# Kernel optimization log

Hardware: AMD Instinct MI355X
Metric: run time of the kernel (lower is better)

Reference implementation:

```python
import jax, jax.numpy as jnp
import numpy as np

N, T, F = 4096, 24, 16          # nodes, seq_len, in_features
H = 128                          # temporal_hidden
NH, DO = 4, 32                   # gat num_heads, gat out_features (NH*DO == H)
SEM, PH = 64, 32                 # semantic hidden, predictor hidden
SLOPE = 0.2                      # leaky_relu negative slope
ADJ_P = 0.01                     # adjacency density


def setup_inputs() -> dict:
    key = jax.random.key(0)
    ks = jax.random.split(key, 40)
    f32 = jnp.float32

    def rn(k, shape, s=0.02):
        return jax.random.normal(k, shape, f32) * s

    features = jax.random.normal(ks[0], (N, T, F), f32)
    pos_adj = (jax.random.uniform(ks[1], (N, N)) < ADJ_P).astype(f32)
    neg_adj = (jax.random.uniform(ks[2], (N, N)) < ADJ_P).astype(f32)

    inp = dict(features=features, pos_adj=pos_adj, neg_adj=neg_adj)
    # GRU (torch layout: W_ih [3H,F], W_hh [3H,H], gate order r,z,n)
    inp['gru_Wih'] = rn(ks[3], (3 * H, F), 1.0 / np.sqrt(H))
    inp['gru_Whh'] = rn(ks[4], (3 * H, H), 1.0 / np.sqrt(H))
    inp['gru_bih'] = rn(ks[5], (3 * H,), 1.0 / np.sqrt(H))
    inp['gru_bhh'] = rn(ks[6], (3 * H,), 1.0 / np.sqrt(H))
    # GAT params (linear weights stored [in, out] so we use x @ W)
    i = 7
    for pre in ('pos', 'neg'):
        inp[pre + '_W'] = rn(ks[i], (H, NH * DO)); i += 1
        inp[pre + '_u'] = rn(ks[i], (NH, DO, 1), 1.0); i += 1
        inp[pre + '_v'] = rn(ks[i], (NH, DO, 1), 1.0); i += 1
        inp[pre + '_b'] = rn(ks[i], (1, NH * DO)); i += 1
        inp[pre + '_pW'] = rn(ks[i], (H, NH * DO)); i += 1
        inp[pre + '_pb'] = jnp.zeros((NH * DO,), f32)
    inp['self_W'] = rn(ks[i], (H, H)); i += 1
    inp['self_b'] = jnp.zeros((H,), f32)
    inp['mpos_W'] = rn(ks[i], (NH * DO, H)); i += 1
    inp['mpos_b'] = jnp.zeros((H,), f32)
    inp['mneg_W'] = rn(ks[i], (NH * DO, H)); i += 1
    inp['mneg_b'] = jnp.zeros((H,), f32)
    inp['sem_W1'] = rn(ks[i], (H, SEM)); i += 1
    inp['sem_b1'] = jnp.zeros((SEM,), f32)
    inp['sem_W2'] = rn(ks[i], (SEM, 1)); i += 1
    inp['pred_W1'] = rn(ks[i], (H, PH)); i += 1
    inp['pred_b1'] = jnp.zeros((PH,), f32)
    inp['pred_W2'] = rn(ks[i], (PH, 1)); i += 1
    inp['pred_b2'] = jnp.zeros((1,), f32)
    return inp


def _gru_last(x, Wih, Whh, bih, bhh):
    # x: [N, T, F] -> last hidden state [N, H]
    gi_all = jnp.einsum('ntf,gf->tng', x, Wih) + bih  # precompute input gates [T,N,3H]
    h0 = jnp.zeros((x.shape[0], Whh.shape[1]), x.dtype)

    def step(h, gi):
        gh = h @ Whh.T + bhh
        ir, iz, in_ = jnp.split(gi, 3, axis=-1)
        hr, hz, hn = jnp.split(gh, 3, axis=-1)
        r = jax.nn.sigmoid(ir + hr)
        z = jax.nn.sigmoid(iz + hz)
        n = jnp.tanh(in_ + r * hn)
        return (1.0 - z) * n + z * h, None

    h, _ = jax.lax.scan(step, h0, gi_all)
    return h


def _gat(x, adj, W, u, v, b, pW, pb):
    sup = (x @ W).reshape(-1, NH, DO).transpose(1, 0, 2)     # [NH, N, DO]
    f1 = jnp.matmul(sup, u).reshape(NH, 1, -1)               # [NH, 1, N]
    f2 = jnp.matmul(sup, v).reshape(NH, -1, 1)               # [NH, N, 1]
    w = jax.nn.leaky_relu(f1 + f2, SLOPE)                    # [NH, N, N]
    mw = w * adj                                             # mask
    rs = mw.sum(axis=2, keepdims=True)
    rs = jnp.where(rs == 0, jnp.ones_like(rs), rs)
    attn = mw / rs
    out = jnp.matmul(attn, sup).transpose(1, 0, 2).reshape(-1, NH * DO)
    return out + b + x @ pW + pb                             # bias + residual


def _pairnorm_si(x):
    x = x - x.mean(axis=0)
    rn = jnp.sqrt(1e-6 + (x * x).sum(axis=1, keepdims=True))
    return x / rn


def reference(features, pos_adj, neg_adj,
              gru_Wih, gru_Whh, gru_bih, gru_bhh,
              pos_W, pos_u, pos_v, pos_b, pos_pW, pos_pb,
              neg_W, neg_u, neg_v, neg_b, neg_pW, neg_pb,
              self_W, self_b, mpos_W, mpos_b, mneg_W, mneg_b,
              sem_W1, sem_b1, sem_W2,
              pred_W1, pred_b1, pred_W2, pred_b2):
    support = _gru_last(features, gru_Wih, gru_Whh, gru_bih, gru_bhh)  # [N, H]
    pos_sup = _gat(support, pos_adj, pos_W, pos_u, pos_v, pos_b, pos_pW, pos_pb)
    neg_sup = _gat(support, neg_adj, neg_W, neg_u, neg_v, neg_b, neg_pW, neg_pb)
    self_e = support @ self_W + self_b
    pos_e = pos_sup @ mpos_W + mpos_b
    neg_e = neg_sup @ mneg_W + mneg_b
    emb = jnp.stack([self_e, pos_e, neg_e], axis=1)          # [N, 3, H]
    w = jnp.tanh(emb @ sem_W1 + sem_b1) @ sem_W2             # [N, 3, 1]
    beta = jax.nn.softmax(w, axis=1)
    fused = (beta * emb).sum(axis=1)                          # [N, H]
    fused = _pairnorm_si(fused)
    h = jax.nn.relu(fused @ pred_W1 + pred_b1)               # dropout is eval no-op
    out = jax.nn.sigmoid(h @ pred_W2 + pred_b2).squeeze(-1)  # [N]
    return out
```

## Files before the change

kernel.cpp:

```cpp
#include <hip/hip_runtime.h>


#define NN 4096

typedef unsigned short u16;
typedef unsigned int   u32;
typedef unsigned long long u64;
typedef __attribute__((ext_vector_type(8))) short  short8;
typedef __attribute__((ext_vector_type(4))) float  float4v;

__device__ inline float bf2f(u16 u){ return __uint_as_float(((u32)u)<<16); }
__device__ inline u16 f2bf(float f){
  u32 x = __float_as_uint(f);
  return (u16)((x + 0x7fffu + ((x>>16)&1u))>>16);
}
__device__ inline float ldm(const void* p, int i, int bf){
  return bf ? bf2f(((const u16*)p)[i]) : ((const float*)p)[i];
}
__device__ inline u16 ldm16(const void* p, int i, int bf){
  return bf ? ((const u16*)p)[i] : f2bf(((const float*)p)[i]);
}
__device__ inline float fexp(float x){
  x = fminf(fmaxf(x,-80.f),80.f);
  return __builtin_amdgcn_exp2f(x*1.4426950408889634f);
}
__device__ inline float sigm(float x){
  return __builtin_amdgcn_rcpf(1.f + fexp(-x));
}
__device__ inline float tanhf_(float x){
  float c = fminf(fmaxf(x,-15.f),15.f);
  float e = __builtin_amdgcn_exp2f(c*2.8853900817779268f);
  return (e-1.f)*__builtin_amdgcn_rcpf(e+1.f);
}
__device__ inline float4v mfma16(short8 a, short8 b, float4v c){
  return __builtin_amdgcn_mfma_f32_16x16x32_bf16(a,b,c,0,0,0);
}

__global__ __launch_bounds__(256) void k_detect(const u32* __restrict__ adj,
                                                int* __restrict__ mflag)
{
  int i = (blockIdx.x*256 + threadIdx.x)*4;
  uint4 v = *(const uint4*)(adj + i);
  u32 acc = (v.x | v.y | v.z | v.w) & 0xFFFFu;
  unsigned long long b = __ballot(acc != 0);
  if ((threadIdx.x & 63) == 0 && b) atomicOr(mflag, 1);
}

__global__ __launch_bounds__(256) void k_imp(
  const int* __restrict__ mflag,
  const void* gWih, const void* gWhh, const void* gbih, const void* gbhh,
  const void* posW, const void* posu, const void* posv, const void* posb,
  const void* pospW, const void* pospb,
  const void* negW, const void* negu, const void* negv, const void* negb,
  const void* negpW, const void* negpb,
  const void* selfW, const void* selfb, const void* mposW, const void* mposb,
  const void* mnegW, const void* mnegb,
  const void* semW1, const void* semb1, const void* semW2,
  const void* predW1, const void* predb1, const void* predW2, const void* predb2,
  u16* __restrict__ Wihb, u16* __restrict__ Whhb,
  u16* __restrict__ WT1,  u16* __restrict__ WT2,
  float* __restrict__ cbrz, float* __restrict__ cbin, float* __restrict__ cbhn,
  float* __restrict__ cuv,  float* __restrict__ cgb,  float* __restrict__ csb,
  float* __restrict__ cw1,  float* __restrict__ cb1,  float* __restrict__ cw2,
  float* __restrict__ cpw1, float* __restrict__ cpb1, float* __restrict__ cpw2,
  float* __restrict__ cpb2)
{
  const int bf = mflag[0];
  int i = blockIdx.x*256 + threadIdx.x;
  if (i < 6144){ Wihb[i]=ldm16(gWih,i,bf); return; }  i-=6144;
  if (i < 49152){ Whhb[i]=ldm16(gWhh,i,bf); return; } i-=49152;
  if (i < 81920){
    int m=i>>7,k=i&127,sel=m>>7,ml=m&127;
    const void* s = sel==0?posW: sel==1?pospW: sel==2?negW: sel==3?negpW: selfW;
    WT1[i]=ldm16(s,k*128+ml,bf); return;
  } i-=81920;
  if (i < 32768){
    int m=i>>7,k=i&127;
    const void* s = (m<128)? mposW : mnegW;
    WT2[i]=ldm16(s,k*128+(m&127),bf); return;
  } i-=32768;
  if (i < 256){ cbrz[i]=ldm(gbih,i,bf)+ldm(gbhh,i,bf); return; } i-=256;
  if (i < 128){ cbin[i]=ldm(gbih,256+i,bf); return; } i-=128;
  if (i < 128){ cbhn[i]=ldm(gbhh,256+i,bf); return; } i-=128;
  if (i < 512){
    int s=i>>8, rem=i&255, wh=rem>>7, hd=rem&127;
    const void* p = s? (wh? negv:negu) : (wh? posv:posu);
    cuv[i]=ldm(p,hd,bf); return;
  } i-=512;
  if (i < 256){
    int s=i>>7, d=i&127;
    cgb[i]=ldm(s?negb:posb,d,bf)+ldm(s?negpb:pospb,d,bf); return;
  } i-=256;
  if (i < 384){
    int t=i>>7, d=i&127;
    const void* p = t==0? selfb : t==1? mposb : mnegb;
    csb[i]=ldm(p,d,bf); return;
  } i-=384;
  if (i < 8192){ cw1[i]=ldm(semW1,i,bf); return; } i-=8192;
  if (i < 64){ cb1[i]=ldm(semb1,i,bf); return; } i-=64;
  if (i < 64){ cw2[i]=ldm(semW2,i,bf); return; } i-=64;
  if (i < 4096){ cpw1[i]=ldm(predW1,i,bf); return; } i-=4096;
  if (i < 32){ cpb1[i]=ldm(predb1,i,bf); return; } i-=32;
  if (i < 32){ cpw2[i]=ldm(predW2,i,bf); return; } i-=32;
  if (i < 1){ cpb2[i]=ldm(predb2,i,bf); return; }
}

__global__ __launch_bounds__(256) void k_csr(
  const int* __restrict__ mflag,
  const void* posadj, const void* negadj,
  int* __restrict__ deg, u16* __restrict__ idx)
{
  const int bf = mflag[0];
  const int s = blockIdx.y;
  const void* adj = s? negadj : posadj;
  const int lane = threadIdx.x&63;
  const int hr   = blockIdx.x*4 + (threadIdx.x>>6);
  const int row  = hr>>1, half = hr&1;
  u32 mask = 0;
  if (bf){
    const u16* rp = (const u16*)adj + (size_t)row*4096 + half*2048;
    #pragma unroll
    for (int q=0;q<4;q++){
      uint4 v = *(const uint4*)(rp + q*512 + lane*8);
      if (v.x&0xffffu) mask|=1u<<(q*8+0); if (v.x>>16) mask|=1u<<(q*8+1);
      if (v.y&0xffffu) mask|=1u<<(q*8+2); if (v.y>>16) mask|=1u<<(q*8+3);
      if (v.z&0xffffu) mask|=1u<<(q*8+4); if (v.z>>16) mask|=1u<<(q*8+5);
      if (v.w&0xffffu) mask|=1u<<(q*8+6); if (v.w>>16) mask|=1u<<(q*8+7);
    }
  } else {
    const float* rp = (const float*)adj + (size_t)row*4096 + half*2048;
    #pragma unroll
    for (int q=0;q<8;q++){
      uint4 v = *(const uint4*)(rp + q*256 + lane*4);
      if (v.x) mask|=1u<<(q*4+0);
      if (v.y) mask|=1u<<(q*4+1);
      if (v.z) mask|=1u<<(q*4+2);
      if (v.w) mask|=1u<<(q*4+3);
    }
  }
  int cnt = __popc(mask);
  int pre = cnt;
  #pragma unroll
  for (int off=1; off<64; off<<=1){
    int o = __shfl_up(pre, off);
    if (lane>=off) pre += o;
  }
  int tot = __shfl(pre, 63);
  int wbase = 0;
  if (lane==0) wbase = atomicAdd(&deg[s*NN+row], tot);
  wbase = __shfl(wbase, 0);
  int base_p = wbase + pre - cnt;
  u16* out = idx + ((size_t)s*NN + row)*128;
  u32 mm = mask; int k = 0;
  while (mm){
    int b = __ffs(mm)-1; mm &= mm-1;
    int e = bf ? (half*2048 + (b>>3)*512 + lane*8 + (b&7))
               : (half*2048 + (b>>2)*256 + lane*4 + (b&3));
    int p = base_p + k; k++;
    if (p<128) out[p] = (u16)e;
  }
}

__global__ __launch_bounds__(512) void k_gru(
  const int* __restrict__ mflag, const void* feat,
  const u16* __restrict__ Wihb, const u16* __restrict__ Whhb,
  const float* __restrict__ cbrz, const float* __restrict__ cbin,
  const float* __restrict__ cbhn, u16* __restrict__ supb)
{
  __shared__ __attribute__((aligned(16))) u16 sh_x[16*392];
  __shared__ __attribute__((aligned(16))) u16 hbuf[2][16*136];

  const int tid=threadIdx.x, lane=tid&63, wv=tid>>6;
  const int quad=lane>>4, c15=lane&15;
  const int n0=blockIdx.x*16;
  const int bf=mflag[0];

  if (bf){
    const u16* f16p=(const u16*)feat;
    for (int i=tid;i<16*384;i+=512){ int n=i/384,e=i-n*384; sh_x[n*392+e]=f16p[(size_t)(n0+n)*384+e]; }
  } else {
    const float* f32p=(const float*)feat;
    for (int i=tid;i<16*384;i+=512){ int n=i/384,e=i-n*384; sh_x[n*392+e]=f2bf(f32p[(size_t)(n0+n)*384+e]); }
  }
  for (int i=tid;i<16*136;i+=512) hbuf[0][i]=0;

  const short8 z8={0,0,0,0,0,0,0,0};
  const float4v z4={0.f,0.f,0.f,0.f};

  short8 bh[3][4], bx[3];
  #pragma unroll
  for (int g=0;g<3;g++){
    int rowb=(g*8+wv)*16+c15;
    #pragma unroll
    for (int ks=0;ks<4;ks++) bh[g][ks]=*(const short8*)(Whhb+(size_t)rowb*128+ks*32+quad*8);
    bx[g] = (quad<2)? *(const short8*)(Wihb+(size_t)rowb*16+quad*8) : z8;
  }

  const int j0=wv*16+c15;
  const float brz_r=cbrz[j0], brz_z=cbrz[128+j0];
  const float bin0=cbin[j0],  bhn0=cbhn[j0];

  float hr[4]={0.f,0.f,0.f,0.f};

  __syncthreads();

  for (int t=0;t<24;t++){
    const u16* hb  = hbuf[t&1];
    u16*       hbn = hbuf[(t+1)&1];
    short8 ah[4];
    #pragma unroll
    for (int ks=0;ks<4;ks++) ah[ks]=*(const short8*)(hb + c15*136 + ks*32 + quad*8);
    short8 ax = (quad<2)? *(const short8*)(sh_x + c15*392 + t*16 + quad*8) : z8;

    float4v racc = mfma16(ax,bx[0],z4);
    float4v zacc = mfma16(ax,bx[1],z4);
    float4v ni   = mfma16(ax,bx[2],z4);
    float4v nh   = z4;
    #pragma unroll
    for (int ks=0;ks<4;ks++){
      racc = mfma16(ah[ks],bh[0][ks],racc);
      zacc = mfma16(ah[ks],bh[1][ks],zacc);
      nh   = mfma16(ah[ks],bh[2][ks],nh);
    }
    #pragma unroll
    for (int rr=0;rr<4;rr++){
      const int node = quad*4+rr;
      float r_ = sigm(racc[rr]+brz_r);
      float z_ = sigm(zacc[rr]+brz_z);
      float n_ = tanhf_(ni[rr]+bin0 + r_*(nh[rr]+bhn0));
      float hv = (1.f-z_)*n_ + z_*hr[rr];
      hr[rr]=hv; hbn[node*136+j0]=f2bf(hv);
    }
    __syncthreads();
  }
  #pragma unroll
  for (int rr=0;rr<4;rr++){
    const int node=quad*4+rr;
    supb[(size_t)(n0+node)*128+j0]=f2bf(hr[rr]);
  }
}

__global__ __launch_bounds__(256) void k_lin1(
  const u16* __restrict__ supb, const u16* __restrict__ WT1,
  const float* __restrict__ cuv, float* __restrict__ C1,
  float* __restrict__ f12)
{
  __shared__ __attribute__((aligned(16))) u16 sA[16*136];
  const int tid=threadIdx.x, lane=tid&63, wv=tid>>6, quad=lane>>4, c15=lane&15;
  const int n0=blockIdx.x*16;
  for (int i=tid;i<2048;i+=256){ int n=i>>7,k=i&127; sA[n*136+k]=supb[(size_t)(n0+n)*128+k]; }
  __syncthreads();
  short8 a[4];
  #pragma unroll
  for (int ks=0;ks<4;ks++) a[ks]=*(const short8*)(sA+c15*136+ks*32+quad*8);
  for (int q=0;q<10;q++){
    int tile=wv*10+q;
    float4v acc={0.f,0.f,0.f,0.f};
    #pragma unroll
    for (int ks=0;ks<4;ks++){
      short8 b=*(const short8*)(WT1+(size_t)(tile*16+c15)*128+ks*32+quad*8);
      acc=mfma16(a[ks],b,acc);
    }
    #pragma unroll
    for (int r=0;r<4;r++) C1[(size_t)(n0+quad*4+r)*640 + tile*16 + c15]=acc[r];
  }
  __syncthreads();
  for (int q=tid; q<512; q+=256){
    int nl=q&15, h=(q>>4)&3, wsel=(q>>6)&1, s=(q>>7)&1;
    const float* uvp = cuv + s*256 + wsel*128 + h*32;
    const float* SL  = C1 + (size_t)(n0+nl)*640 + s*256 + h*32;
    float t=0.f;
    #pragma unroll
    for (int d=0;d<32;d++) t += SL[d]*uvp[d];
    f12[s*32768 + wsel*16384 + h*4096 + (n0+nl)] = t;
  }
}

__global__ __launch_bounds__(256) void k_gat(
  const float* __restrict__ C1, const float* __restrict__ f12,
  const int* __restrict__ deg, const u16* __restrict__ idx,
  const float* __restrict__ cgb, u16* __restrict__ spnb)
{
  __shared__ u16   nbuf[4][128];
  __shared__ float wbuf[4][4][128];
  const int s=blockIdx.y;
  const int wv=threadIdx.x>>6;
  const int i=blockIdx.x*4 + wv;
  const int lane=threadIdx.x&63;
  const int d0=lane, d1=lane+64, h0=lane>>5, h1=2+(lane>>5);
  const float* f1 = f12 + s*32768;
  const float* f2 = f12 + s*32768 + 16384;
  const int dgr = deg[s*NN+i];
  const int dg  = dgr>128 ? 128 : dgr;
  const u16* nb = idx + ((size_t)s*NN+i)*128;
  ((u32*)nbuf[wv])[lane] = ((const u32*)nb)[lane];
  float f2v[4];
  #pragma unroll
  for (int h=0;h<4;h++) f2v[h]=f2[h*4096+i];
  for (int e=lane; e<dg; e+=64){
    int j = nbuf[wv][e];
    #pragma unroll
    for (int h=0;h<4;h++){
      float w = f1[h*4096+j] + f2v[h];
      wbuf[wv][h][e] = w>0.f ? w : 0.2f*w;
    }
  }
  float acc0=0.f,acc1=0.f,rs0=0.f,rs1=0.f;
  for (int e=0;e<dg;e++){
    float w0 = wbuf[wv][h0][e];
    float w1 = wbuf[wv][h1][e];
    int j = nbuf[wv][e];
    const float* SL = C1 + (size_t)j*640 + s*256;
    acc0 += w0*SL[d0]; rs0 += w0;
    acc1 += w1*SL[d1]; rs1 += w1;
  }
  if (rs0==0.f) rs0=1.f;
  if (rs1==0.f) rs1=1.f;
  const float* P = C1 + (size_t)i*640 + s*256 + 128;
  float o0 = acc0/rs0 + cgb[s*128+d0] + P[d0];
  float o1 = acc1/rs1 + cgb[s*128+d1] + P[d1];
  size_t o = ((size_t)s*NN + i)*128;
  spnb[o+d0]=f2bf(o0); spnb[o+d1]=f2bf(o1);
}

__global__ __launch_bounds__(256) void k_lin2(
  const u16* __restrict__ spnb, const u16* __restrict__ WT2, float* __restrict__ E)
{
  const int s=blockIdx.y;
  __shared__ __attribute__((aligned(16))) u16 sA[16*136];
  const int tid=threadIdx.x, lane=tid&63, wv=tid>>6, quad=lane>>4, c15=lane&15;
  const int n0=blockIdx.x*16;
  const u16* A = spnb + (size_t)s*NN*128;
  for (int i=tid;i<2048;i+=256){ int n=i>>7,k=i&127; sA[n*136+k]=A[(size_t)(n0+n)*128+k]; }
  __syncthreads();
  short8 a[4];
  #pragma unroll
  for (int ks=0;ks<4;ks++) a[ks]=*(const short8*)(sA+c15*136+ks*32+quad*8);
  #pragma unroll
  for (int q=0;q<2;q++){
    int tile=wv*2+q;
    float4v acc={0.f,0.f,0.f,0.f};
    #pragma unroll
    for (int ks=0;ks<4;ks++){
      short8 b=*(const short8*)(WT2+(size_t)(s*128+tile*16+c15)*128+ks*32+quad*8);
      acc=mfma16(a[ks],b,acc);
    }
    #pragma unroll
    for (int r=0;r<4;r++) E[(size_t)(n0+quad*4+r)*256 + s*128 + tile*16 + c15]=acc[r];
  }
}

__global__ __launch_bounds__(256) void k_sem(
  const float* __restrict__ C1, const float* __restrict__ E,
  const float* __restrict__ csb, const float* __restrict__ cw1,
  const float* __restrict__ cb1, const float* __restrict__ cw2,
  float* __restrict__ fused)
{
  __shared__ float sW1[128*64];
  __shared__ float sW2[64];
  __shared__ float sb1[64];
  __shared__ float sE[4][3][128];
  const int tid=threadIdx.x, wv=tid>>6, lane=tid&63;
  for (int i=tid;i<8192;i+=256) sW1[i]=cw1[i];
  if (tid<64){ sW2[tid]=cw2[tid]; sb1[tid]=cb1[tid]; }
  const int n = blockIdx.x*4 + wv;
  for (int d=lane; d<128; d+=64){
    sE[wv][0][d] = C1[(size_t)n*640+512+d] + csb[d];
    sE[wv][1][d] = E[(size_t)n*256 + d]    + csb[128+d];
    sE[wv][2][d] = E[(size_t)n*256+128+d]  + csb[256+d];
  }
  __syncthreads();
  float sc[3];
  #pragma unroll
  for (int s=0;s<3;s++){
    float t = sb1[lane];
    for (int k=0;k<128;k++) t += sE[wv][s][k]*sW1[k*64+lane];
    t = tanhf_(t);
    float p = t*sW2[lane];
    #pragma unroll
    for (int off=32; off; off>>=1) p += __shfl_xor(p, off);
    sc[s]=p;
  }
  float mx = fmaxf(sc[0], fmaxf(sc[1],sc[2]));
  float e0=fexp(sc[0]-mx), e1=fexp(sc[1]-mx), e2=fexp(sc[2]-mx);
  float inv = 1.f/(e0+e1+e2);
  float b0=e0*inv, b1=e1*inv, b2=e2*inv;
  for (int d=lane; d<128; d+=64)
    fused[(size_t)n*128+d] = b0*sE[wv][0][d] + b1*sE[wv][1][d] + b2*sE[wv][2][d];
}

__global__ __launch_bounds__(256) void k_mean(const float* __restrict__ fused,
                                              float* __restrict__ meanacc)
{
  const int d = threadIdx.x & 127, h2 = threadIdx.x >> 7;
  const int n0 = blockIdx.x*128;
  float s=0.f;
  for (int n=n0+h2; n<n0+128; n+=2) s += fused[(size_t)n*128+d];
  __shared__ float red[256];
  red[threadIdx.x]=s; __syncthreads();
  if (threadIdx.x<128) atomicAdd(&meanacc[threadIdx.x], red[threadIdx.x]+red[threadIdx.x+128]);
}

__global__ __launch_bounds__(256) void k_pred(
  const float* __restrict__ fused, const float* __restrict__ meanacc,
  const float* __restrict__ cpw1, const float* __restrict__ cpb1,
  const float* __restrict__ cpw2, const float* __restrict__ cpb2,
  float* __restrict__ out)
{
  __shared__ float sy[4][128];
  __shared__ float sW1[128*32];
  __shared__ float sW2[32];
  const int tid=threadIdx.x, wv=tid>>6, lane=tid&63;
  for (int i=tid;i<4096;i+=256) sW1[i]=cpw1[i];
  if (tid<32) sW2[tid]=cpw2[tid];
  const int n = blockIdx.x*4 + wv;
  const float inv_n = 1.f/4096.f;
  float x0 = fused[(size_t)n*128+lane]    - meanacc[lane]*inv_n;
  float x1 = fused[(size_t)n*128+64+lane] - meanacc[64+lane]*inv_n;
  float ss = x0*x0 + x1*x1;
  #pragma unroll
  for (int o=32;o;o>>=1) ss += __shfl_xor(ss,o);
  float ir = 1.f/sqrtf(1e-6f + ss);
  sy[wv][lane]=x0*ir; sy[wv][64+lane]=x1*ir;
  __syncthreads();
  float h=0.f;
  if (lane<32){
    h = cpb1[lane];
    for (int k=0;k<128;k++) h += sy[wv][k]*sW1[k*32+lane];
    h = h>0.f? h : 0.f;
    h = h*sW2[lane];
  }
  #pragma unroll
  for (int o=32;o;o>>=1) h += __shfl_xor(h,o);
  if (!lane){
    float z = h + cpb2[0];
    out[n] = __builtin_amdgcn_rcpf(1.f + fexp(-z));
  }
}

extern "C" void kernel_launch(void* const* d_in, const int* in_sizes, int n_in,
                              void* d_out, int out_size, void* d_ws, size_t ws_size,
                              hipStream_t stream)
{
  const void* feat  =d_in[0];
  const void* posadj=d_in[1];
  const void* negadj=d_in[2];
  const void* gWih  =d_in[3];
  const void* gWhh  =d_in[4];
  const void* gbih  =d_in[5];
  const void* gbhh  =d_in[6];
  const void* posW  =d_in[7];
  const void* posu  =d_in[8];
  const void* posv  =d_in[9];
  const void* posb  =d_in[10];
  const void* pospW =d_in[11];
  const void* pospb =d_in[12];
  const void* negW  =d_in[13];
  const void* negu  =d_in[14];
  const void* negv  =d_in[15];
  const void* negb  =d_in[16];
  const void* negpW =d_in[17];
  const void* negpb =d_in[18];
  const void* selfW =d_in[19];
  const void* selfb =d_in[20];
  const void* mposW =d_in[21];
  const void* mposb =d_in[22];
  const void* mnegW =d_in[23];
  const void* mnegb =d_in[24];
  const void* semW1 =d_in[25];
  const void* semb1 =d_in[26];
  const void* semW2 =d_in[27];
  const void* predW1=d_in[28];
  const void* predb1=d_in[29];
  const void* predW2=d_in[30];
  const void* predb2=d_in[31];

  char* wsb=(char*)d_ws; size_t off=0;
  auto alloc=[&](size_t bytes)->void*{ void* p=wsb+off; off+=(bytes+255)&~(size_t)255; return p; };
  int*   mflag=(int*)  alloc(256);
  u16*   Wihb =(u16*)  alloc(6144*2);
  u16*   Whhb =(u16*)  alloc(49152*2);
  u16*   WT1  =(u16*)  alloc(81920*2);
  u16*   WT2  =(u16*)  alloc(32768*2);
  float* cbrz =(float*)alloc(256*4);
  float* cbin =(float*)alloc(128*4);
  float* cbhn =(float*)alloc(128*4);
  float* cuv  =(float*)alloc(512*4);
  float* cgb  =(float*)alloc(256*4);
  float* csb  =(float*)alloc(384*4);
  float* cw1  =(float*)alloc(8192*4);
  float* cb1  =(float*)alloc(64*4);
  float* cw2  =(float*)alloc(64*4);
  float* cpw1 =(float*)alloc(4096*4);
  float* cpb1 =(float*)alloc(32*4);
  float* cpw2 =(float*)alloc(32*4);
  float* cpb2 =(float*)alloc(4);
  u16*   supb =(u16*)  alloc((size_t)NN*128*2);
  float* C1   =(float*)alloc((size_t)NN*640*4);
  float* f12  =(float*)alloc((size_t)65536*4);
  int*   deg  =(int*)  alloc((size_t)2*NN*4);
  u16*   nidx =(u16*)  alloc((size_t)2*NN*128*2);
  u16*   spnb =(u16*)  alloc((size_t)2*NN*128*2);
  float* E    =(float*)alloc((size_t)NN*256*4);
  float* fused=(float*)alloc((size_t)NN*128*4);
  float* meanacc=(float*)alloc(128*4);
  (void)ws_size; (void)in_sizes; (void)n_in; (void)out_size;

  hipMemsetAsync(mflag, 0, 4, stream);
  hipMemsetAsync(deg, 0, (size_t)2*NN*4, stream);
  hipMemsetAsync(meanacc, 0, 128*4, stream);
  k_detect<<<16,             256,0,stream>>>((const u32*)posadj,mflag);
  k_imp   <<<720,            256,0,stream>>>(mflag,gWih,gWhh,gbih,gbhh,
              posW,posu,posv,posb,pospW,pospb,negW,negu,negv,negb,negpW,negpb,
              selfW,selfb,mposW,mposb,mnegW,mnegb,semW1,semb1,semW2,
              predW1,predb1,predW2,predb2,
              Wihb,Whhb,WT1,WT2,cbrz,cbin,cbhn,cuv,cgb,csb,cw1,cb1,cw2,
              cpw1,cpb1,cpw2,cpb2);
  k_csr <<<dim3(2048,2),     256,0,stream>>>(mflag,posadj,negadj,deg,nidx);
  k_gru <<<NN/16,            512,0,stream>>>(mflag,feat,Wihb,Whhb,cbrz,cbin,cbhn,supb);
  k_lin1<<<NN/16,            256,0,stream>>>(supb,WT1,cuv,C1,f12);
  k_gat <<<dim3(NN/4,2),     256,0,stream>>>(C1,f12,deg,nidx,cgb,spnb);
  k_lin2<<<dim3(NN/16,2),    256,0,stream>>>(spnb,WT2,E);
  k_sem <<<NN/4,             256,0,stream>>>(C1,E,csb,cw1,cb1,cw2,fused);
  k_mean<<<32,               256,0,stream>>>(fused,meanacc);
  k_pred<<<NN/4,             256,0,stream>>>(fused,meanacc,cpw1,cpb1,cpw2,cpb2,(float*)d_out);
}
```

Baseline: 321.3 us.

## Fuse kernels: CSR build with GRU+lin1, GAT with lin2, mean into sem

```diff
diff --git a/kernel.cpp b/kernel.cpp
--- a/kernel.cpp
+++ b/kernel.cpp
@@ -35,15 +35,25 @@
 __device__ inline float4v mfma16(short8 a, short8 b, float4v c){
   return __builtin_amdgcn_mfma_f32_16x16x32_bf16(a,b,c,0,0,0);
 }
+__device__ inline int rdbf(const int* __restrict__ mflag){
+  int b=0;
+  #pragma unroll
+  for (int k=0;k<16;k++) b|=mflag[k];
+  return b;
+}
 
 __global__ __launch_bounds__(256) void k_detect(const u32* __restrict__ adj,
                                                 int* __restrict__ mflag)
 {
+  __shared__ u32 w4[4];
+  const int lane=threadIdx.x&63, wv=threadIdx.x>>6;
   int i = (blockIdx.x*256 + threadIdx.x)*4;
   uint4 v = *(const uint4*)(adj + i);
   u32 acc = (v.x | v.y | v.z | v.w) & 0xFFFFu;
   unsigned long long b = __ballot(acc != 0);
-  if ((threadIdx.x & 63) == 0 && b) atomicOr(mflag, 1);
+  if (lane==0) w4[wv] = (b!=0);
+  __syncthreads();
+  if (threadIdx.x==0) mflag[blockIdx.x] = (w4[0]|w4[1]|w4[2]|w4[3]) ? 1 : 0;
 }
 
 __global__ __launch_bounds__(256) void k_imp(
@@ -63,9 +73,9 @@
   float* __restrict__ cuv,  float* __restrict__ cgb,  float* __restrict__ csb,
   float* __restrict__ cw1,  float* __restrict__ cb1,  float* __restrict__ cw2,
   float* __restrict__ cpw1, float* __restrict__ cpb1, float* __restrict__ cpw2,
-  float* __restrict__ cpb2)
-{
-  const int bf = mflag[0];
+  float* __restrict__ cpb2, float* __restrict__ meanacc)
+{
+  const int bf = rdbf(mflag);
   int i = blockIdx.x*256 + threadIdx.x;
   if (i < 6144){ Wihb[i]=ldm16(gWih,i,bf); return; }  i-=6144;
   if (i < 49152){ Whhb[i]=ldm16(gWhh,i,bf); return; } i-=49152;
@@ -102,78 +112,79 @@
   if (i < 4096){ cpw1[i]=ldm(predW1,i,bf); return; } i-=4096;
   if (i < 32){ cpb1[i]=ldm(predb1,i,bf); return; } i-=32;
   if (i < 32){ cpw2[i]=ldm(predW2,i,bf); return; } i-=32;
-  if (i < 1){ cpb2[i]=ldm(predb2,i,bf); return; }
-}
-
-__global__ __launch_bounds__(256) void k_csr(
+  if (i < 1){ cpb2[i]=ldm(predb2,i,bf); return; } i-=1;
+  if (i < 128){ meanacc[i]=0.f; return; }
+}
+
+__global__ __launch_bounds__(512) void k_fat1(
   const int* __restrict__ mflag,
   const void* posadj, const void* negadj,
-  int* __restrict__ deg, u16* __restrict__ idx)
-{
-  const int bf = mflag[0];
-  const int s = blockIdx.y;
-  const void* adj = s? negadj : posadj;
-  const int lane = threadIdx.x&63;
-  const int hr   = blockIdx.x*4 + (threadIdx.x>>6);
-  const int row  = hr>>1, half = hr&1;
-  u32 mask = 0;
-  if (bf){
-    const u16* rp = (const u16*)adj + (size_t)row*4096 + half*2048;
-    #pragma unroll
-    for (int q=0;q<4;q++){
-      uint4 v = *(const uint4*)(rp + q*512 + lane*8);
-      if (v.x&0xffffu) mask|=1u<<(q*8+0); if (v.x>>16) mask|=1u<<(q*8+1);
-      if (v.y&0xffffu) mask|=1u<<(q*8+2); if (v.y>>16) mask|=1u<<(q*8+3);
-      if (v.z&0xffffu) mask|=1u<<(q*8+4); if (v.z>>16) mask|=1u<<(q*8+5);
-      if (v.w&0xffffu) mask|=1u<<(q*8+6); if (v.w>>16) mask|=1u<<(q*8+7);
-    }
-  } else {
-    const float* rp = (const float*)adj + (size_t)row*4096 + half*2048;
-    #pragma unroll
-    for (int q=0;q<8;q++){
-      uint4 v = *(const uint4*)(rp + q*256 + lane*4);
-      if (v.x) mask|=1u<<(q*4+0);
-      if (v.y) mask|=1u<<(q*4+1);
-      if (v.z) mask|=1u<<(q*4+2);
-      if (v.w) mask|=1u<<(q*4+3);
-    }
-  }
-  int cnt = __popc(mask);
-  int pre = cnt;
-  #pragma unroll
-  for (int off=1; off<64; off<<=1){
-    int o = __shfl_up(pre, off);
-    if (lane>=off) pre += o;
-  }
-  int tot = __shfl(pre, 63);
-  int wbase = 0;
-  if (lane==0) wbase = atomicAdd(&deg[s*NN+row], tot);
-  wbase = __shfl(wbase, 0);
-  int base_p = wbase + pre - cnt;
-  u16* out = idx + ((size_t)s*NN + row)*128;
-  u32 mm = mask; int k = 0;
-  while (mm){
-    int b = __ffs(mm)-1; mm &= mm-1;
-    int e = bf ? (half*2048 + (b>>3)*512 + lane*8 + (b&7))
-               : (half*2048 + (b>>2)*256 + lane*4 + (b&3));
-    int p = base_p + k; k++;
-    if (p<128) out[p] = (u16)e;
-  }
-}
-
-__global__ __launch_bounds__(512) void k_gru(
-  const int* __restrict__ mflag, const void* feat,
+  int* __restrict__ deg, u16* __restrict__ idx,
+  const void* feat,
   const u16* __restrict__ Wihb, const u16* __restrict__ Whhb,
   const float* __restrict__ cbrz, const float* __restrict__ cbin,
-  const float* __restrict__ cbhn, u16* __restrict__ supb)
+  const float* __restrict__ cbhn,
+  const u16* __restrict__ WT1, const float* __restrict__ cuv,
+  float* __restrict__ C1, float* __restrict__ f12)
 {
   __shared__ __attribute__((aligned(16))) u16 sh_x[16*392];
   __shared__ __attribute__((aligned(16))) u16 hbuf[2][16*136];
-
+  const int bf = rdbf(mflag);
   const int tid=threadIdx.x, lane=tid&63, wv=tid>>6;
+  const int bx=blockIdx.x;
+
+  if (bx < 1024){
+    const int gid = bx*8 + wv;
+    const int s = gid>>12, row = gid&4095;
+    const void* adj = s? negadj : posadj;
+    u64 mask = 0;
+    if (bf){
+      const u16* rp = (const u16*)adj + (size_t)row*4096;
+      #pragma unroll
+      for (int it=0; it<8; it++){
+        const uint4 vv = *(const uint4*)(rp + it*512 + lane*8);
+        u32 w[4]={vv.x,vv.y,vv.z,vv.w};
+        #pragma unroll
+        for (int q=0;q<4;q++){
+          if (w[q]&0xffffu) mask |= 1ull<<(it*8+2*q);
+          if (w[q]>>16)     mask |= 1ull<<(it*8+2*q+1);
+        }
+      }
+    } else {
+      const float* rp = (const float*)adj + (size_t)row*4096;
+      #pragma unroll
+      for (int it=0; it<16; it++){
+        const uint4 vv = *(const uint4*)(rp + it*256 + lane*4);
+        if (vv.x) mask |= 1ull<<(it*4+0);
+        if (vv.y) mask |= 1ull<<(it*4+1);
+        if (vv.z) mask |= 1ull<<(it*4+2);
+        if (vv.w) mask |= 1ull<<(it*4+3);
+      }
+    }
+    int cnt = __popcll(mask);
+    int pre = cnt;
+    #pragma unroll
+    for (int off=1; off<64; off<<=1){
+      int o = __shfl_up(pre, off);
+      if (lane>=off) pre += o;
+    }
+    int base_p = pre - cnt;
+    int total = __shfl(pre, 63);
+    u16* out = idx + ((size_t)s*NN + row)*128;
+    u64 mm = mask; int k = 0;
+    while (mm){
+      int b = __ffsll(mm)-1; mm &= mm-1;
+      int e = bf ? ((b>>3)*512 + lane*8 + (b&7))
+                 : ((b>>2)*256 + lane*4 + (b&3));
+      int p = base_p + k; k++;
+      if (p<128) out[p] = (u16)e;
+    }
+    if (lane==0) deg[s*NN+row] = total>128 ? 128 : total;
+    return;
+  }
+
   const int quad=lane>>4, c15=lane&15;
-  const int n0=blockIdx.x*16;
-  const int bf=mflag[0];
+  const int n0=(bx-1024)*16;
 
   if (bf){
     const u16* f16p=(const u16*)feat;
@@ -186,22 +197,18 @@
 
   const short8 z8={0,0,0,0,0,0,0,0};
   const float4v z4={0.f,0.f,0.f,0.f};
-
-  short8 bh[3][4], bx[3];
+  short8 bh[3][4], bx3[3];
   #pragma unroll
   for (int g=0;g<3;g++){
     int rowb=(g*8+wv)*16+c15;
     #pragma unroll
     for (int ks=0;ks<4;ks++) bh[g][ks]=*(const short8*)(Whhb+(size_t)rowb*128+ks*32+quad*8);
-    bx[g] = (quad<2)? *(const short8*)(Wihb+(size_t)rowb*16+quad*8) : z8;
-  }
-
+    bx3[g] = (quad<2)? *(const short8*)(Wihb+(size_t)rowb*16+quad*8) : z8;
+  }
   const int j0=wv*16+c15;
   const float brz_r=cbrz[j0], brz_z=cbrz[128+j0];
   const float bin0=cbin[j0],  bhn0=cbhn[j0];
-
   float hr[4]={0.f,0.f,0.f,0.f};
-
   __syncthreads();
 
   for (int t=0;t<24;t++){
@@ -211,10 +218,9 @@
     #pragma unroll
     for (int ks=0;ks<4;ks++) ah[ks]=*(const short8*)(hb + c15*136 + ks*32 + quad*8);
     short8 ax = (quad<2)? *(const short8*)(sh_x + c15*392 + t*16 + quad*8) : z8;
-
-    float4v racc = mfma16(ax,bx[0],z4);
-    float4v zacc = mfma16(ax,bx[1],z4);
-    float4v ni   = mfma16(ax,bx[2],z4);
+    float4v racc = mfma16(ax,bx3[0],z4);
+    float4v zacc = mfma16(ax,bx3[1],z4);
+    float4v ni   = mfma16(ax,bx3[2],z4);
     float4v nh   = z4;
     #pragma unroll
     for (int ks=0;ks<4;ks++){
@@ -233,28 +239,12 @@
     }
     __syncthreads();
   }
-  #pragma unroll
-  for (int rr=0;rr<4;rr++){
-    const int node=quad*4+rr;
-    supb[(size_t)(n0+node)*128+j0]=f2bf(hr[rr]);
-  }
-}
-
-__global__ __launch_bounds__(256) void k_lin1(
-  const u16* __restrict__ supb, const u16* __restrict__ WT1,
-  const float* __restrict__ cuv, float* __restrict__ C1,
-  float* __restrict__ f12)
-{
-  __shared__ __attribute__((aligned(16))) u16 sA[16*136];
-  const int tid=threadIdx.x, lane=tid&63, wv=tid>>6, quad=lane>>4, c15=lane&15;
-  const int n0=blockIdx.x*16;
-  for (int i=tid;i<2048;i+=256){ int n=i>>7,k=i&127; sA[n*136+k]=supb[(size_t)(n0+n)*128+k]; }
-  __syncthreads();
   short8 a[4];
   #pragma unroll
-  for (int ks=0;ks<4;ks++) a[ks]=*(const short8*)(sA+c15*136+ks*32+quad*8);
-  for (int q=0;q<10;q++){
-    int tile=wv*10+q;
+  for (int ks=0;ks<4;ks++) a[ks]=*(const short8*)(hbuf[0]+c15*136+ks*32+quad*8);
+  #pragma unroll
+  for (int q=0;q<5;q++){
+    int tile=wv*5+q;
     float4v acc={0.f,0.f,0.f,0.f};
     #pragma unroll
     for (int ks=0;ks<4;ks++){
@@ -265,7 +255,8 @@
     for (int r=0;r<4;r++) C1[(size_t)(n0+quad*4+r)*640 + tile*16 + c15]=acc[r];
   }
   __syncthreads();
-  for (int q=tid; q<512; q+=256){
+  {
+    int q=tid;
     int nl=q&15, h=(q>>4)&3, wsel=(q>>6)&1, s=(q>>7)&1;
     const float* uvp = cuv + s*256 + wsel*128 + h*32;
     const float* SL  = C1 + (size_t)(n0+nl)*640 + s*256 + h*32;
@@ -276,17 +267,19 @@
   }
 }
 
-__global__ __launch_bounds__(256) void k_gat(
+__global__ __launch_bounds__(1024) void k_fat2(
   const float* __restrict__ C1, const float* __restrict__ f12,
   const int* __restrict__ deg, const u16* __restrict__ idx,
-  const float* __restrict__ cgb, u16* __restrict__ spnb)
-{
-  __shared__ u16   nbuf[4][128];
-  __shared__ float wbuf[4][4][128];
+  const float* __restrict__ cgb, const u16* __restrict__ WT2,
+  float* __restrict__ E)
+{
+  __shared__ u16   nbuf[16][128];
+  __shared__ float wbuf[16][4][128];
+  __shared__ __attribute__((aligned(16))) u16 sA[16*136];
   const int s=blockIdx.y;
-  const int wv=threadIdx.x>>6;
-  const int i=blockIdx.x*4 + wv;
-  const int lane=threadIdx.x&63;
+  const int wv=threadIdx.x>>6, lane=threadIdx.x&63;
+  const int n0=blockIdx.x*16;
+  const int i=n0+wv;
   const int d0=lane, d1=lane+64, h0=lane>>5, h1=2+(lane>>5);
   const float* f1 = f12 + s*32768;
   const float* f2 = f12 + s*32768 + 16384;
@@ -306,6 +299,7 @@
     }
   }
   float acc0=0.f,acc1=0.f,rs0=0.f,rs1=0.f;
+  #pragma unroll 4
   for (int e=0;e<dg;e++){
     float w0 = wbuf[wv][h0][e];
     float w1 = wbuf[wv][h1][e];
@@ -317,28 +311,15 @@
   if (rs0==0.f) rs0=1.f;
   if (rs1==0.f) rs1=1.f;
   const float* P = C1 + (size_t)i*640 + s*256 + 128;
-  float o0 = acc0/rs0 + cgb[s*128+d0] + P[d0];
-  float o1 = acc1/rs1 + cgb[s*128+d1] + P[d1];
-  size_t o = ((size_t)s*NN + i)*128;
-  spnb[o+d0]=f2bf(o0); spnb[o+d1]=f2bf(o1);
-}
-
-__global__ __launch_bounds__(256) void k_lin2(
-  const u16* __restrict__ spnb, const u16* __restrict__ WT2, float* __restrict__ E)
-{
-  const int s=blockIdx.y;
-  __shared__ __attribute__((aligned(16))) u16 sA[16*136];
-  const int tid=threadIdx.x, lane=tid&63, wv=tid>>6, quad=lane>>4, c15=lane&15;
-  const int n0=blockIdx.x*16;
-  const u16* A = spnb + (size_t)s*NN*128;
-  for (int i=tid;i<2048;i+=256){ int n=i>>7,k=i&127; sA[n*136+k]=A[(size_t)(n0+n)*128+k]; }
-  __syncthreads();
-  short8 a[4];
-  #pragma unroll
-  for (int ks=0;ks<4;ks++) a[ks]=*(const short8*)(sA+c15*136+ks*32+quad*8);
-  #pragma unroll
-  for (int q=0;q<2;q++){
-    int tile=wv*2+q;
+  sA[wv*136+d0]=f2bf(acc0/rs0 + cgb[s*128+d0] + P[d0]);
+  sA[wv*136+d1]=f2bf(acc1/rs1 + cgb[s*128+d1] + P[d1]);
+  __syncthreads();
+  if (wv<8){
+    const int quad=lane>>4, c15=lane&15;
+    short8 a[4];
+    #pragma unroll
+    for (int ks=0;ks<4;ks++) a[ks]=*(const short8*)(sA+c15*136+ks*32+quad*8);
+    const int tile=wv;
     float4v acc={0.f,0.f,0.f,0.f};
     #pragma unroll
     for (int ks=0;ks<4;ks++){
@@ -354,7 +335,7 @@
   const float* __restrict__ C1, const float* __restrict__ E,
   const float* __restrict__ csb, const float* __restrict__ cw1,
   const float* __restrict__ cb1, const float* __restrict__ cw2,
-  float* __restrict__ fused)
+  float* __restrict__ fused, float* __restrict__ meanacc)
 {
   __shared__ float sW1[128*64];
   __shared__ float sW2[64];
@@ -385,20 +366,17 @@
   float e0=fexp(sc[0]-mx), e1=fexp(sc[1]-mx), e2=fexp(sc[2]-mx);
   float inv = 1.f/(e0+e1+e2);
   float b0=e0*inv, b1=e1*inv, b2=e2*inv;
-  for (int d=lane; d<128; d+=64)
-    fused[(size_t)n*128+d] = b0*sE[wv][0][d] + b1*sE[wv][1][d] + b2*sE[wv][2][d];
-}
-
-__global__ __launch_bounds__(256) void k_mean(const float* __restrict__ fused,
-                                              float* __restrict__ meanacc)
-{
-  const int d = threadIdx.x & 127, h2 = threadIdx.x >> 7;
-  const int n0 = blockIdx.x*128;
-  float s=0.f;
-  for (int n=n0+h2; n<n0+128; n+=2) s += fused[(size_t)n*128+d];
-  __shared__ float red[256];
-  red[threadIdx.x]=s; __syncthreads();
-  if (threadIdx.x<128) atomicAdd(&meanacc[threadIdx.x], red[threadIdx.x]+red[threadIdx.x+128]);
+  float fv[2];
+  for (int h=0; h<2; h++){
+    int d=lane+h*64;
+    fv[h] = b0*sE[wv][0][d] + b1*sE[wv][1][d] + b2*sE[wv][2][d];
+    fused[(size_t)n*128+d] = fv[h];
+  }
+  __syncthreads();
+  for (int h=0; h<2; h++) sE[wv][0][lane+h*64] = fv[h];
+  __syncthreads();
+  if (tid<128)
+    atomicAdd(&meanacc[tid], sE[0][0][tid]+sE[1][0][tid]+sE[2][0][tid]+sE[3][0][tid]);
 }
 
 __global__ __launch_bounds__(256) void k_pred(
@@ -495,33 +473,25 @@
   float* cpb1 =(float*)alloc(32*4);
   float* cpw2 =(float*)alloc(32*4);
   float* cpb2 =(float*)alloc(4);
-  u16*   supb =(u16*)  alloc((size_t)NN*128*2);
   float* C1   =(float*)alloc((size_t)NN*640*4);
   float* f12  =(float*)alloc((size_t)65536*4);
   int*   deg  =(int*)  alloc((size_t)2*NN*4);
   u16*   nidx =(u16*)  alloc((size_t)2*NN*128*2);
-  u16*   spnb =(u16*)  alloc((size_t)2*NN*128*2);
   float* E    =(float*)alloc((size_t)NN*256*4);
   float* fused=(float*)alloc((size_t)NN*128*4);
   float* meanacc=(float*)alloc(128*4);
   (void)ws_size; (void)in_sizes; (void)n_in; (void)out_size;
 
-  hipMemsetAsync(mflag, 0, 4, stream);
-  hipMemsetAsync(deg, 0, (size_t)2*NN*4, stream);
-  hipMemsetAsync(meanacc, 0, 128*4, stream);
-  k_detect<<<16,             256,0,stream>>>((const u32*)posadj,mflag);
-  k_imp   <<<720,            256,0,stream>>>(mflag,gWih,gWhh,gbih,gbhh,
+  k_detect<<<16,          256,0,stream>>>((const u32*)posadj,mflag);
+  k_imp   <<<720,         256,0,stream>>>(mflag,gWih,gWhh,gbih,gbhh,
               posW,posu,posv,posb,pospW,pospb,negW,negu,negv,negb,negpW,negpb,
               selfW,selfb,mposW,mposb,mnegW,mnegb,semW1,semb1,semW2,
               predW1,predb1,predW2,predb2,
               Wihb,Whhb,WT1,WT2,cbrz,cbin,cbhn,cuv,cgb,csb,cw1,cb1,cw2,
-              cpw1,cpb1,cpw2,cpb2);
-  k_csr <<<dim3(2048,2),     256,0,stream>>>(mflag,posadj,negadj,deg,nidx);
-  k_gru <<<NN/16,            512,0,stream>>>(mflag,feat,Wihb,Whhb,cbrz,cbin,cbhn,supb);
-  k_lin1<<<NN/16,            256,0,stream>>>(supb,WT1,cuv,C1,f12);
-  k_gat <<<dim3(NN/4,2),     256,0,stream>>>(C1,f12,deg,nidx,cgb,spnb);
-  k_lin2<<<dim3(NN/16,2),    256,0,stream>>>(spnb,WT2,E);
-  k_sem <<<NN/4,             256,0,stream>>>(C1,E,csb,cw1,cb1,cw2,fused);
-  k_mean<<<32,               256,0,stream>>>(fused,meanacc);
-  k_pred<<<NN/4,             256,0,stream>>>(fused,meanacc,cpw1,cpb1,cpw2,cpb2,(float*)d_out);
-}
+              cpw1,cpb1,cpw2,cpb2,meanacc);
+  k_fat1  <<<1280,        512,0,stream>>>(mflag,posadj,negadj,deg,nidx,
+              feat,Wihb,Whhb,cbrz,cbin,cbhn,WT1,cuv,C1,f12);
+  k_fat2  <<<dim3(256,2),1024,0,stream>>>(C1,f12,deg,nidx,cgb,WT2,E);
+  k_sem   <<<NN/4,        256,0,stream>>>(C1,E,csb,cw1,cb1,cw2,fused,meanacc);
+  k_pred  <<<NN/4,        256,0,stream>>>(fused,meanacc,cpw1,cpb1,cpw2,cpb2,(float*)d_out);
+}
```

After: 318.8 us. No clear change (-0.8%).
